# Kernel optimization log

Hardware: AMD Instinct MI355X
Metric: run time of the kernel (lower is better)

Reference implementation:

```python
import jax, jax.numpy as jnp
import numpy as np

N_EMBD = 1024
N_HEAD = 16
HEAD_DIM = N_EMBD // N_HEAD


def setup_inputs() -> dict:
    key = jax.random.key(0)
    ks = jax.random.split(key, 5)
    scale = 0.02
    x = jax.random.normal(ks[0], (2, 2048, N_EMBD), dtype=jnp.float32)
    w_attn = jax.random.normal(ks[1], (N_EMBD, 3 * N_EMBD), dtype=jnp.float32) * scale
    b_attn = jax.random.normal(ks[2], (3 * N_EMBD,), dtype=jnp.float32) * scale
    w_proj = jax.random.normal(ks[3], (N_EMBD, N_EMBD), dtype=jnp.float32) * scale
    b_proj = jax.random.normal(ks[4], (N_EMBD,), dtype=jnp.float32) * scale
    return {"x": x, "w_attn": w_attn, "b_attn": b_attn, "w_proj": w_proj, "b_proj": b_proj}


def reference(x, w_attn, b_attn, w_proj, b_proj):
    B, T, C = x.shape
    qkv = x @ w_attn + b_attn  # [B,T,3C]
    q, k, v = jnp.split(qkv, 3, axis=-1)
    # [B, H, T, D]
    q = q.reshape(B, T, N_HEAD, HEAD_DIM).transpose(0, 2, 1, 3)
    k = k.reshape(B, T, N_HEAD, HEAD_DIM).transpose(0, 2, 1, 3)
    v = v.reshape(B, T, N_HEAD, HEAD_DIM).transpose(0, 2, 1, 3)
    att = jnp.einsum("bhqd,bhkd->bhqk", q, k) * (1.0 / np.sqrt(HEAD_DIM))
    causal = jnp.tril(jnp.ones((T, T), dtype=bool))
    att = jnp.where(causal[None, None], att, jnp.float32(-jnp.inf))
    att = jax.nn.softmax(att, axis=-1)
    y = jnp.einsum("bhqk,bhkd->bhqd", att, v)  # [B,H,T,D]
    y = y.transpose(0, 2, 1, 3).reshape(B, T, C)
    return y @ w_proj + b_proj
```

## Files before the change

kernel.cpp:

```cpp
#include <hip/hip_runtime.h>
#include <stdint.h>

#define SEQ   2048
#define EMBD  1024
#define M_ROWS 4096

typedef unsigned short u16;
typedef unsigned int u32;
typedef __attribute__((ext_vector_type(8))) short bf16x8;
typedef __attribute__((ext_vector_type(4))) float f32x4;

__device__ __forceinline__ u16 f2b(float f) {
  u32 x = __float_as_uint(f);
  return (u16)((x + 0x7FFFu + ((x >> 16) & 1u)) >> 16);
}

__device__ __forceinline__ u32 pkbf(float a, float b) {
  u32 r;
  asm("v_cvt_pk_bf16_f32 %0, %1, %2" : "=v"(r) : "v"(a), "v"(b));
  return r;
}

__device__ __forceinline__ float exp2fast(float x) {
#if __has_builtin(__builtin_amdgcn_exp2f)
  return __builtin_amdgcn_exp2f(x);
#else
  return __expf(x * 0.69314718f);
#endif
}

__device__ __forceinline__ float rcpfast(float x) {
#if __has_builtin(__builtin_amdgcn_rcpf)
  return __builtin_amdgcn_rcpf(x);
#else
  return 1.f / x;
#endif
}

#define AS1(p) ((const __attribute__((address_space(1))) void*)(uintptr_t)(p))
#define AS3(p) ((__attribute__((address_space(3))) void*)(uintptr_t)(p))

__global__ __launch_bounds__(256) void cvt_f32_bf16(
    const float* __restrict__ in, u16* __restrict__ out, int n8) {
  int i = blockIdx.x * 256 + threadIdx.x;
  if (i >= n8) return;
  const float4* p = (const float4*)in + 2 * (size_t)i;
  float4 a = p[0], b = p[1];
  uint4 o;
  o.x = (u32)f2b(a.x) | ((u32)f2b(a.y) << 16);
  o.y = (u32)f2b(a.z) | ((u32)f2b(a.w) << 16);
  o.z = (u32)f2b(b.x) | ((u32)f2b(b.y) << 16);
  o.w = (u32)f2b(b.z) | ((u32)f2b(b.w) << 16);
  ((uint4*)out)[i] = o;
}

__global__ __launch_bounds__(256) void transpose_cvt(
    const float* __restrict__ w, u16* __restrict__ wt, int K, int N) {
  __shared__ float t[64][65];
  const int n0 = blockIdx.x * 64, k0 = blockIdx.y * 64;
  const int c = threadIdx.x & 63, r4 = threadIdx.x >> 6;
#pragma unroll
  for (int j = 0; j < 16; ++j) {
    const int r = j * 4 + r4;
    t[c][r] = w[(size_t)(k0 + r) * N + n0 + c];
  }
  __syncthreads();
#pragma unroll
  for (int j = 0; j < 16; ++j) {
    const int nr = j * 4 + r4;
    wt[(size_t)(n0 + nr) * K + k0 + c] = f2b(t[nr][c]);
  }
}

template <bool OUT_BF16>
__global__ __launch_bounds__(256) void gemm_kmajor(
    const u16* __restrict__ A, const u16* __restrict__ Bt,
    const float* __restrict__ bias, void* __restrict__ outp,
    int M, int N, int K, int nbx) {
  __shared__ __align__(16) u16 As[128 * 32];
  __shared__ __align__(16) u16 Bs[128 * 32];

  const int nwg = gridDim.x;
  const int qq = nwg >> 3, rr = nwg & 7;
  const int xcd = blockIdx.x & 7, off = blockIdx.x >> 3;
  const int wgid = (xcd < rr ? xcd * (qq + 1) : rr * (qq + 1) + (xcd - rr) * qq) + off;
  const int bx = wgid % nbx, by = wgid / nbx;
  const int row0 = by * 128, col0 = bx * 128;

  const int tid = threadIdx.x;
  const int w = tid >> 6, lane = tid & 63;
  const int wrow = (w >> 1) * 64, wcol = (w & 1) * 64;

  f32x4 acc[4][4];
#pragma unroll
  for (int a = 0; a < 4; ++a)
#pragma unroll
    for (int b = 0; b < 4; ++b)
#pragma unroll
      for (int e = 0; e < 4; ++e) acc[a][b][e] = 0.f;

  const size_t Kb = (size_t)K * 2;

  for (int k0 = 0; k0 < K; k0 += 32) {
#pragma unroll
    for (int c = 0; c < 4; ++c) {
      const int ch = w * 4 + c;
      const int i = ch & 7;
      const int rloc = i * 16 + (lane >> 2);
      const int kb = ((lane & 3) * 16) ^ ((rloc & 3) << 4);
      const char* src;
      char* dst;
      if (ch < 8) {
        src = (const char*)A + (size_t)(row0 + rloc) * Kb + k0 * 2 + kb;
        dst = (char*)As + i * 1024;
      } else {
        src = (const char*)Bt + (size_t)(col0 + rloc) * Kb + k0 * 2 + kb;
        dst = (char*)Bs + i * 1024;
      }
      __builtin_amdgcn_global_load_lds(AS1(src), AS3(dst), 16, 0, 0);
    }
    __syncthreads();

    bf16x8 af[4], bf[4];
#pragma unroll
    for (int rb = 0; rb < 4; ++rb) {
      const int rl = wrow + rb * 16 + (lane & 15);
      const int kb2 = ((lane >> 4) * 16) ^ ((rl & 3) << 4);
      af[rb] = *(const bf16x8*)((const char*)As + rl * 64 + kb2);
    }
#pragma unroll
    for (int cb = 0; cb < 4; ++cb) {
      const int rl = wcol + cb * 16 + (lane & 15);
      const int kb2 = ((lane >> 4) * 16) ^ ((rl & 3) << 4);
      bf[cb] = *(const bf16x8*)((const char*)Bs + rl * 64 + kb2);
    }
#pragma unroll
    for (int rb = 0; rb < 4; ++rb)
#pragma unroll
      for (int cb = 0; cb < 4; ++cb)
        acc[rb][cb] = __builtin_amdgcn_mfma_f32_16x16x32_bf16(
            af[rb], bf[cb], acc[rb][cb], 0, 0, 0);
    __syncthreads();
  }

#pragma unroll
  for (int cb = 0; cb < 4; ++cb) {
    const int colg = col0 + wcol + cb * 16 + (lane & 15);
    const float bv = bias[colg];
#pragma unroll
    for (int rb = 0; rb < 4; ++rb) {
#pragma unroll
      for (int i = 0; i < 4; ++i) {
        const int rowg = row0 + wrow + rb * 16 + (lane >> 4) * 4 + i;
        const float v = acc[rb][cb][i] + bv;
        if (OUT_BF16) {
          const u32 hv = f2b(v);
          const u32 pv = (u32)__shfl_xor((int)hv, 1);
          if (!(lane & 1))
            *(u32*)((u16*)outp + (size_t)rowg * N + colg) = hv | (pv << 16);
        } else {
          ((float*)outp)[(size_t)rowg * N + colg] = v;
        }
      }
    }
  }
}

__global__ __launch_bounds__(256, 2) void attn_mfma2(
    const u16* __restrict__ qkvb, u16* __restrict__ yb) {
  __shared__ __align__(16) char lds[32768];

  const int bx = blockIdx.x;
  const int pr = bx >> 5;
  const int bh = bx & 31;
  const int bb = bh >> 4, h = bh & 15;

  const int tid = threadIdx.x;
  const int w = tid >> 6, lane = tid & 63;
  const int hh = lane >> 4, qh = lane & 15;

  const size_t rowb = 6144;
  const char* base = (const char*)qkvb + (size_t)bb * SEQ * rowb;
  const int koffb = EMBD * 2 + h * 128;
  const int voffb = 2 * EMBD * 2 + h * 128;

  const int krow_in_chunk = lane >> 3;
  const int vkv = (tid & 31) * 2;
  const int vdg = tid >> 5;

  for (int half = 0; half < 2; ++half) {
    const int qt = half ? pr : 31 - pr;
    const int q_abs = qt * 64 + w * 16 + qh;
    const int qloc = w * 16 + qh;

    const char* qp = base + (size_t)q_abs * rowb + h * 128 + hh * 16;
    const bf16x8 qf0 = *(const bf16x8*)qp;
    const bf16x8 qf1 = *(const bf16x8*)(qp + 64);

    float m2 = -1e30f, l = 0.f;
    f32x4 of[4];
#pragma unroll
    for (int db = 0; db < 4; ++db)
#pragma unroll
      for (int e = 0; e < 4; ++e) of[db][e] = 0.f;

    {
#pragma unroll
      for (int cc = 0; cc < 2; ++cc) {
        const int i = w * 2 + cc;
        const int kvl = i * 8 + krow_in_chunk;
        const int gs = (lane & 7) ^ ((i & 3) | ((krow_in_chunk & 1) << 2));
        const char* src = base + (size_t)kvl * rowb + koffb + gs * 16;
        __builtin_amdgcn_global_load_lds(AS1(src), AS3(lds + i * 1024), 16, 0, 0);
      }
      const char* vp = base + (size_t)vkv * rowb + voffb + vdg * 16;
      uint4 va = *(const uint4*)vp;
      uint4 vb = *(const uint4*)(vp + rowb);
      union { uint4 q; u16 s[8]; } ua, ub;
      ua.q = va; ub.q = vb;
      u32* vt = (u32*)(lds + 16384);
#pragma unroll
      for (int e = 0; e < 8; ++e) {
        const int d = vdg * 8 + e;
        vt[d * 32 + ((vkv >> 1) ^ ((d & 7) << 2))] =
            (u32)ua.s[e] | ((u32)ub.s[e] << 16);
      }
    }
    __syncthreads();

    for (int kt = 0; kt <= qt; ++kt) {
      const int cur = kt & 1;
      const char* ksb = lds + cur * 8192;
      const char* vtb = lds + 16384 + cur * 8192;

      uint4 va, vb;
      const bool pref = (kt < qt);
      if (pref) {
#pragma unroll
        for (int cc = 0; cc < 2; ++cc) {
          const int i = w * 2 + cc;
          const int kvl = i * 8 + krow_in_chunk;
          const int gs = (lane & 7) ^ ((i & 3) | ((krow_in_chunk & 1) << 2));
          const char* src =
              base + (size_t)((kt + 1) * 64 + kvl) * rowb + koffb + gs * 16;
          __builtin_amdgcn_global_load_lds(
              AS1(src), AS3(lds + (cur ^ 1) * 8192 + i * 1024), 16, 0, 0);
        }
        const char* vp =
            base + (size_t)((kt + 1) * 64 + vkv) * rowb + voffb + vdg * 16;
        va = *(const uint4*)vp;
        vb = *(const uint4*)(vp + rowb);
      }

      f32x4 st[4];
#pragma unroll
      for (int rb = 0; rb < 4; ++rb) {
#pragma unroll
        for (int e = 0; e < 4; ++e) st[rb][e] = 0.f;
        const int kv = 32 * (rb >> 1) + 8 * ((lane >> 2) & 3) + 4 * (rb & 1) +
                       (lane & 3);
        const int f = ((kv >> 3) & 3) | ((kv & 1) << 2);
        const char* rp = ksb + kv * 128;
        const bf16x8 k0 = *(const bf16x8*)(rp + ((hh * 16) ^ (f << 4)));
        const bf16x8 k1 = *(const bf16x8*)(rp + ((64 + hh * 16) ^ (f << 4)));
        st[rb] = __builtin_amdgcn_mfma_f32_16x16x32_bf16(k0, qf0, st[rb], 0, 0, 0);
        st[rb] = __builtin_amdgcn_mfma_f32_16x16x32_bf16(k1, qf1, st[rb], 0, 0, 0);
      }

      const float C = 0.18033688f;
      float pmax = -3.0e38f;
      if (kt == qt) {
#pragma unroll
        for (int rb = 0; rb < 4; ++rb) {
          const int kvb = 32 * (rb >> 1) + 8 * hh + 4 * (rb & 1);
#pragma unroll
          for (int i = 0; i < 4; ++i) {
            float v = st[rb][i] * C;
            if (kvb + i > qloc) v = -3.0e38f;
            st[rb][i] = v;
            pmax = fmaxf(pmax, v);
          }
        }
      } else {
#pragma unroll
        for (int rb = 0; rb < 4; ++rb)
#pragma unroll
          for (int i = 0; i < 4; ++i) {
            const float v = st[rb][i] * C;
            st[rb][i] = v;
            pmax = fmaxf(pmax, v);
          }
      }
      pmax = fmaxf(pmax, __shfl_xor(pmax, 16));
      pmax = fmaxf(pmax, __shfl_xor(pmax, 32));

      if (__any(pmax > m2 + 5.f)) {
        const float mn = fmaxf(m2, pmax);
        const float al = exp2fast(m2 - mn);
        m2 = mn;
        l *= al;
#pragma unroll
        for (int db = 0; db < 4; ++db)
#pragma unroll
          for (int e = 0; e < 4; ++e) of[db][e] *= al;
      }

      float ls = 0.f;
#pragma unroll
      for (int rb = 0; rb < 4; ++rb)
#pragma unroll
        for (int i = 0; i < 4; ++i) {
          const float p = exp2fast(st[rb][i] - m2);
          st[rb][i] = p;
          ls += p;
        }
      ls += __shfl_xor(ls, 16);
      ls += __shfl_xor(ls, 32);
      l += ls;

      union { u32 wd[4]; bf16x8 v; } pf0, pf1;
      pf0.wd[0] = pkbf(st[0][0], st[0][1]);
      pf0.wd[1] = pkbf(st[0][2], st[0][3]);
      pf0.wd[2] = pkbf(st[1][0], st[1][1]);
      pf0.wd[3] = pkbf(st[1][2], st[1][3]);
      pf1.wd[0] = pkbf(st[2][0], st[2][1]);
      pf1.wd[1] = pkbf(st[2][2], st[2][3]);
      pf1.wd[2] = pkbf(st[3][0], st[3][1]);
      pf1.wd[3] = pkbf(st[3][2], st[3][3]);

#pragma unroll
      for (int db = 0; db < 4; ++db) {
        const int d = db * 16 + qh;
        const int g = d & 7;
        const char* rp = vtb + d * 128;
        const bf16x8 v0 = *(const bf16x8*)(rp + ((hh * 16) ^ (g << 4)));
        const bf16x8 v1 = *(const bf16x8*)(rp + ((64 + hh * 16) ^ (g << 4)));
        of[db] = __builtin_amdgcn_mfma_f32_16x16x32_bf16(v0, pf0.v, of[db], 0, 0, 0);
        of[db] = __builtin_amdgcn_mfma_f32_16x16x32_bf16(v1, pf1.v, of[db], 0, 0, 0);
      }

      if (pref) {
        union { uint4 q; u16 s[8]; } ua, ub;
        ua.q = va; ub.q = vb;
        u32* vt = (u32*)(lds + 16384 + (cur ^ 1) * 8192);
#pragma unroll
        for (int e = 0; e < 8; ++e) {
          const int d = vdg * 8 + e;
          vt[d * 32 + ((vkv >> 1) ^ ((d & 7) << 2))] =
              (u32)ua.s[e] | ((u32)ub.s[e] << 16);
        }
      }
      __syncthreads();
    }

    const float inv = rcpfast(l);
    u16* yrow = yb + (size_t)(bb * SEQ + q_abs) * EMBD + h * 64;
#pragma unroll
    for (int db = 0; db < 4; ++db) {
      const u32 w0 = pkbf(of[db][0] * inv, of[db][1] * inv);
      const u32 w1 = pkbf(of[db][2] * inv, of[db][3] * inv);
      *(u32*)(yrow + db * 16 + 4 * hh) = w0;
      *(u32*)(yrow + db * 16 + 4 * hh + 2) = w1;
    }
    __syncthreads();
  }
}

extern "C" void kernel_launch(void* const* d_in, const int* in_sizes, int n_in,
                              void* d_out, int out_size, void* d_ws,
                              size_t ws_size, hipStream_t stream) {
  const float* x      = (const float*)d_in[0];
  const float* w_attn = (const float*)d_in[1];
  const float* b_attn = (const float*)d_in[2];
  const float* w_proj = (const float*)d_in[3];
  const float* b_proj = (const float*)d_in[4];
  float* out = (float*)d_out;

  u16* xb   = (u16*)d_ws;
  u16* wat  = xb + (size_t)M_ROWS * EMBD;
  u16* wpt  = wat + (size_t)3 * EMBD * EMBD;
  u16* qkvb = wpt + (size_t)EMBD * EMBD;
  u16* yb   = qkvb + (size_t)M_ROWS * 3 * EMBD;

  cvt_f32_bf16<<<(M_ROWS * EMBD / 8 + 255) / 256, 256, 0, stream>>>(
      x, xb, M_ROWS * EMBD / 8);
  transpose_cvt<<<dim3(3 * EMBD / 64, EMBD / 64), 256, 0, stream>>>(
      w_attn, wat, EMBD, 3 * EMBD);
  transpose_cvt<<<dim3(EMBD / 64, EMBD / 64), 256, 0, stream>>>(
      w_proj, wpt, EMBD, EMBD);

  gemm_kmajor<true><<<768, 256, 0, stream>>>(
      xb, wat, b_attn, qkvb, M_ROWS, 3 * EMBD, EMBD, 24);

  attn_mfma2<<<512, 256, 0, stream>>>(qkvb, yb);

  gemm_kmajor<false><<<256, 256, 0, stream>>>(
      yb, wpt, b_proj, out, M_ROWS, EMBD, EMBD, 8);
}
```

Measured before the change: 207.7 us.

## Double-buffer GEMM LDS tiles, merge weight transposes, raise MFMA wave priority

The GEMM now keeps two LDS buffers and issues the next K-tile's global-to-LDS loads before computing the current tile, so load latency can overlap MFMA work with one barrier per iteration. The two weight transpose-convert launches are merged into one launch with a combined grid, saving a kernel launch. The attention kernel wraps its MFMA sections in s_setprio to favour waves issuing matrix ops. Double buffering doubles GEMM LDS use (32KB per block), which may reduce occupancy.

```diff
diff --git a/kernel.cpp b/kernel.cpp
--- a/kernel.cpp
+++ b/kernel.cpp
@@ -54,10 +54,17 @@
   ((uint4*)out)[i] = o;
 }
 
-__global__ __launch_bounds__(256) void transpose_cvt(
-    const float* __restrict__ w, u16* __restrict__ wt, int K, int N) {
+__global__ __launch_bounds__(256) void transpose_cvt2(
+    const float* __restrict__ wa, u16* __restrict__ wat,
+    const float* __restrict__ wp, u16* __restrict__ wpt) {
   __shared__ float t[64][65];
-  const int n0 = blockIdx.x * 64, k0 = blockIdx.y * 64;
+  const int bxr = blockIdx.x;
+  const float* w = (bxr < 48) ? wa : wp;
+  u16* wt = (bxr < 48) ? wat : wpt;
+  const int N = (bxr < 48) ? 3072 : 1024;
+  const int bx = (bxr < 48) ? bxr : bxr - 48;
+  const int K = 1024;
+  const int n0 = bx * 64, k0 = blockIdx.y * 64;
   const int c = threadIdx.x & 63, r4 = threadIdx.x >> 6;
 #pragma unroll
   for (int j = 0; j < 16; ++j) {
@@ -77,8 +84,7 @@
     const u16* __restrict__ A, const u16* __restrict__ Bt,
     const float* __restrict__ bias, void* __restrict__ outp,
     int M, int N, int K, int nbx) {
-  __shared__ __align__(16) u16 As[128 * 32];
-  __shared__ __align__(16) u16 Bs[128 * 32];
+  __shared__ __align__(16) u16 sm[2][2][128 * 32];
 
   const int nwg = gridDim.x;
   const int qq = nwg >> 3, rr = nwg & 7;
@@ -101,47 +107,56 @@
 
   const size_t Kb = (size_t)K * 2;
 
-  for (int k0 = 0; k0 < K; k0 += 32) {
+  auto stage = [&](int k0, int buf) {
 #pragma unroll
     for (int c = 0; c < 4; ++c) {
       const int ch = w * 4 + c;
       const int i = ch & 7;
       const int rloc = i * 16 + (lane >> 2);
       const int kb = ((lane & 3) * 16) ^ ((rloc & 3) << 4);
-      const char* src;
-      char* dst;
-      if (ch < 8) {
-        src = (const char*)A + (size_t)(row0 + rloc) * Kb + k0 * 2 + kb;
-        dst = (char*)As + i * 1024;
-      } else {
-        src = (const char*)Bt + (size_t)(col0 + rloc) * Kb + k0 * 2 + kb;
-        dst = (char*)Bs + i * 1024;
-      }
+      const u16* mat = (ch < 8) ? A : Bt;
+      const int r0 = (ch < 8) ? row0 : col0;
+      const char* src = (const char*)mat + (size_t)(r0 + rloc) * Kb + k0 * 2 + kb;
+      char* dst = (char*)&sm[buf][(ch < 8) ? 0 : 1][0] + i * 1024;
       __builtin_amdgcn_global_load_lds(AS1(src), AS3(dst), 16, 0, 0);
     }
-    __syncthreads();
-
-    bf16x8 af[4], bf[4];
+  };
+
+  auto compute = [&](int buf) {
+    bf16x8 af[4], bfr[4];
+    const char* As = (const char*)&sm[buf][0][0];
+    const char* Bs = (const char*)&sm[buf][1][0];
 #pragma unroll
     for (int rb = 0; rb < 4; ++rb) {
       const int rl = wrow + rb * 16 + (lane & 15);
       const int kb2 = ((lane >> 4) * 16) ^ ((rl & 3) << 4);
-      af[rb] = *(const bf16x8*)((const char*)As + rl * 64 + kb2);
+      af[rb] = *(const bf16x8*)(As + rl * 64 + kb2);
     }
 #pragma unroll
     for (int cb = 0; cb < 4; ++cb) {
       const int rl = wcol + cb * 16 + (lane & 15);
       const int kb2 = ((lane >> 4) * 16) ^ ((rl & 3) << 4);
-      bf[cb] = *(const bf16x8*)((const char*)Bs + rl * 64 + kb2);
+      bfr[cb] = *(const bf16x8*)(Bs + rl * 64 + kb2);
     }
 #pragma unroll
     for (int rb = 0; rb < 4; ++rb)
 #pragma unroll
       for (int cb = 0; cb < 4; ++cb)
         acc[rb][cb] = __builtin_amdgcn_mfma_f32_16x16x32_bf16(
-            af[rb], bf[cb], acc[rb][cb], 0, 0, 0);
+            af[rb], bfr[cb], acc[rb][cb], 0, 0, 0);
+  };
+
+  const int nt = K >> 5;
+  stage(0, 0);
+  int cur = 0;
+  for (int t = 0; t < nt - 1; ++t) {
     __syncthreads();
+    stage((t + 1) * 32, cur ^ 1);
+    compute(cur);
+    cur ^= 1;
   }
+  __syncthreads();
+  compute(cur);
 
 #pragma unroll
   for (int cb = 0; cb < 4; ++cb) {
@@ -253,6 +268,7 @@
       }
 
       f32x4 st[4];
+      __builtin_amdgcn_s_setprio(1);
 #pragma unroll
       for (int rb = 0; rb < 4; ++rb) {
 #pragma unroll
@@ -266,6 +282,7 @@
         st[rb] = __builtin_amdgcn_mfma_f32_16x16x32_bf16(k0, qf0, st[rb], 0, 0, 0);
         st[rb] = __builtin_amdgcn_mfma_f32_16x16x32_bf16(k1, qf1, st[rb], 0, 0, 0);
       }
+      __builtin_amdgcn_s_setprio(0);
 
       const float C = 0.18033688f;
       float pmax = -3.0e38f;
@@ -328,6 +345,7 @@
       pf1.wd[2] = pkbf(st[3][0], st[3][1]);
       pf1.wd[3] = pkbf(st[3][2], st[3][3]);
 
+      __builtin_amdgcn_s_setprio(1);
 #pragma unroll
       for (int db = 0; db < 4; ++db) {
         const int d = db * 16 + qh;
@@ -338,6 +356,7 @@
         of[db] = __builtin_amdgcn_mfma_f32_16x16x32_bf16(v0, pf0.v, of[db], 0, 0, 0);
         of[db] = __builtin_amdgcn_mfma_f32_16x16x32_bf16(v1, pf1.v, of[db], 0, 0, 0);
       }
+      __builtin_amdgcn_s_setprio(0);
 
       if (pref) {
         union { uint4 q; u16 s[8]; } ua, ub;
@@ -384,10 +403,7 @@
 
   cvt_f32_bf16<<<(M_ROWS * EMBD / 8 + 255) / 256, 256, 0, stream>>>(
       x, xb, M_ROWS * EMBD / 8);
-  transpose_cvt<<<dim3(3 * EMBD / 64, EMBD / 64), 256, 0, stream>>>(
-      w_attn, wat, EMBD, 3 * EMBD);
-  transpose_cvt<<<dim3(EMBD / 64, EMBD / 64), 256, 0, stream>>>(
-      w_proj, wpt, EMBD, EMBD);
+  transpose_cvt2<<<dim3(64, 16), 256, 0, stream>>>(w_attn, wat, w_proj, wpt);
 
   gemm_kmajor<true><<<768, 256, 0, stream>>>(
       xb, wat, b_attn, qkvb, M_ROWS, 3 * EMBD, EMBD, 24);
```

Result: faster. 188.2 us (-9.4%).
